# Kernel tuning notes

Measured on AMD Instinct MI355X. Metric: run time of the kernel, lower is better.

Reference implementation:

```python
import jax, jax.numpy as jnp
import numpy as np

H, KV, D, HID, Q, S = 16, 8, 128, 2048, 1024, 8192
CACHE_POS = 4096

def rotate_half(x, axis):
    x1, x2 = jnp.split(x, 2, axis)
    return jnp.concatenate((-x2, x1), axis=axis)

def setup_inputs() -> dict:
    key = jax.random.key(0)
    ks = jax.random.split(key, 12)
    hidden_states = jax.random.normal(ks[0], (1, HID, 1, Q), jnp.float32)
    # RoPE tables for the new token positions [CACHE_POS, CACHE_POS+Q)
    pos = jnp.arange(CACHE_POS, CACHE_POS + Q, dtype=jnp.float32)
    inv_freq = 1.0 / (10000.0 ** (jnp.arange(0, D, 2, dtype=jnp.float32) / D))
    ang = pos[:, None] * inv_freq[None, :]                      # (Q, D/2)
    cos = jnp.tile(jnp.cos(ang), (1, 2))[None, None]            # (1,1,Q,D)
    sin = jnp.tile(jnp.sin(ang), (1, 2))[None, None]
    cos_t = jnp.transpose(cos, (0, 1, 3, 2))                    # (1,1,D,Q)
    sin_t = jnp.transpose(sin, (0, 1, 3, 2))
    # causal mask over full cache: key slot s visible to query i iff s <= CACHE_POS + i
    k_idx = jnp.arange(S)[:, None]
    q_idx = jnp.arange(Q)[None, :]
    attention_mask = jnp.where(k_idx <= CACHE_POS + q_idx, 0.0, -1e9).astype(jnp.float32)[None, None]  # (1,1,S,Q)
    key_cache = 0.02 * jax.random.normal(ks[1], (1, KV, S, D), jnp.float32)
    value_cache = 0.02 * jax.random.normal(ks[2], (1, KV, S, D), jnp.float32)
    w = lambda k, shp: 0.02 * jax.random.normal(k, shp, jnp.float32)
    return dict(hidden_states=hidden_states, cos=cos, sin=sin, cos_t=cos_t, sin_t=sin_t,
                attention_mask=attention_mask, key_cache=key_cache, value_cache=value_cache,
                Wq=w(ks[3], (HID, HID)), bq=w(ks[4], (HID,)),
                Wk=w(ks[5], (KV * D, HID)), bk=w(ks[6], (KV * D,)),
                Wv=w(ks[7], (KV * D, HID)), bv=w(ks[8], (KV * D,)),
                Wo=w(ks[9], (HID, HID)), cache_position=CACHE_POS)

def reference(hidden_states, cos, sin, cos_t, sin_t, attention_mask,
              key_cache, value_cache, Wq, bq, Wk, bk, Wv, bv, Wo, cache_position):
    # 1x1-conv style projections on channels-first (1, C, 1, Q)
    q = jnp.einsum('oc,bcxq->boxq', Wq, hidden_states) + bq[None, :, None, None]
    k = jnp.einsum('oc,bcxq->boxq', Wk, hidden_states) + bk[None, :, None, None]
    v = jnp.einsum('oc,bcxq->boxq', Wv, hidden_states) + bv[None, :, None, None]
    q = q.reshape(1, H, D, Q)                                   # (1,H,D,Q)
    k = k.reshape(1, KV, D, Q).transpose(0, 1, 3, 2)            # (1,KV,Q,D)
    v = v.reshape(1, KV, D, Q).transpose(0, 1, 3, 2)
    # inline RoPE: q along head_dim axis (-2), k along last axis
    q = q * cos_t + rotate_half(q, -2) * sin_t
    k = k * cos + rotate_half(k, -1) * sin
    # KV-cache scatter at layer_idx=0, offset cache_position
    key_cache = jax.lax.dynamic_update_slice(key_cache, k, (0, 0, cache_position, 0))
    value_cache = jax.lax.dynamic_update_slice(value_cache, v, (0, 0, cache_position, 0))
    k_all = key_cache[0]                                        # (KV,S,D)
    v_all = value_cache[0]
    qg = q.reshape(KV, H // KV, D, Q)                           # GQA groups
    scores = jnp.einsum('ksd,kgdq->kgsq', k_all, qg) / jnp.sqrt(jnp.float32(D))
    scores = scores + attention_mask[0]                         # (1,S,Q) broadcast
    w = jax.nn.softmax(scores, axis=2)                          # softmax over cache slots
    out = jnp.einsum('kgsq,ksd->kgdq', w, v_all)                # (KV,G,D,Q)
    out = out.reshape(1, H * D, 1, Q)
    attn_output = jnp.einsum('oc,bcxq->boxq', Wo, out)
    return attn_output
```

## Files before the change

kernel.cpp:

```cpp
#include <hip/hip_runtime.h>

#define H_HEADS 16
#define KV_HEADS 8
#define DHEAD 128
#define HID 2048
#define NQ 1024
#define SCACHE 8192
#define CPOS 4096
#define SEFF 5120

typedef __attribute__((ext_vector_type(8))) __bf16 bf16x8;
typedef __attribute__((ext_vector_type(4))) float f32x4;
typedef unsigned short u16;
typedef unsigned int u32;

__device__ __forceinline__ u16 f2b(float f) {
  u32 u = __float_as_uint(f);
  u += 0x7fffu + ((u >> 16) & 1u);
  return (u16)(u >> 16);
}
__device__ __forceinline__ u16 f2b_t(float f) {
  return (u16)(__float_as_uint(f) >> 16);
}
__device__ __forceinline__ float b2f(u16 b) { return __uint_as_float(((u32)b) << 16); }
__device__ __forceinline__ u32 pk2(u16 a, u16 b) { return (u32)a | ((u32)b << 16); }
__device__ __forceinline__ uint2 f4b4(float4 v) {
  uint2 o;
  o.x = pk2(f2b(v.x), f2b(v.y));
  o.y = pk2(f2b(v.z), f2b(v.w));
  return o;
}

union U4 { uint4 v; u16 u[8]; };

__global__ void __launch_bounds__(256) k_conv_w(const float* __restrict__ Wq,
                                                const float* __restrict__ Wk,
                                                const float* __restrict__ Wv,
                                                u16* __restrict__ Wb) {
  int i = blockIdx.x * 256 + threadIdx.x;
  const float* src;
  int off;
  if (i < 1048576) { src = Wq; off = i; }
  else if (i < 1572864) { src = Wk; off = i - 1048576; }
  else { src = Wv; off = i - 1572864; }
  float4 v = ((const float4*)src)[off];
  *(uint2*)(Wb + (size_t)i * 4) = f4b4(v);
}

__global__ void __launch_bounds__(256) k_f32_to_bf16(const float* __restrict__ src,
                                                     u16* __restrict__ dst, int n4) {
  int i = blockIdx.x * 256 + threadIdx.x;
  if (i < n4) {
    float4 v = ((const float4*)src)[i];
    *(uint2*)(dst + (size_t)i * 4) = f4b4(v);
  }
}

__global__ void __launch_bounds__(256) k_transpose_h(const float* __restrict__ hid,
                                                     u16* __restrict__ hT) {
  __shared__ __align__(16) float ls[64 * 68];
  int t = threadIdx.x;
  int c0 = blockIdx.x * 64, q0 = blockIdx.y * 64;
#pragma unroll
  for (int it = 0; it < 4; ++it) {
    int c = it * 256 + t;
    int row = c >> 4, ch = c & 15;
    *(float4*)(ls + row * 68 + ch * 4) =
        *(const float4*)(hid + (size_t)(c0 + row) * NQ + q0 + ch * 4);
  }
  __syncthreads();
  int ql = t & 63, cch = t >> 6;
  u32 ob[8];
#pragma unroll
  for (int j = 0; j < 8; ++j)
    ob[j] = pk2(f2b(ls[(cch * 16 + 2 * j) * 68 + ql]), f2b(ls[(cch * 16 + 2 * j + 1) * 68 + ql]));
  uint4* dst = (uint4*)(hT + (size_t)(q0 + ql) * HID + c0 + cch * 16);
  dst[0] = make_uint4(ob[0], ob[1], ob[2], ob[3]);
  dst[1] = make_uint4(ob[4], ob[5], ob[6], ob[7]);
}

__global__ void __launch_bounds__(256) k_prep_vT(const float* __restrict__ vc,
                                                 u16* __restrict__ vT) {
  __shared__ __align__(16) float ls[64 * 132];
  int t = threadIdx.x;
  int s0 = blockIdx.x * 64;
  int kv = blockIdx.y;
#pragma unroll
  for (int it = 0; it < 8; ++it) {
    int c = it * 256 + t;
    int row = c >> 5, ch = c & 31;
    *(float4*)(ls + row * 132 + ch * 4) =
        *(const float4*)(vc + ((size_t)kv * SCACHE + s0 + row) * DHEAD + ch * 4);
  }
  __syncthreads();
  int d = t >> 1, sch = t & 1;
  u32 ob[16];
#pragma unroll
  for (int j = 0; j < 16; ++j)
    ob[j] = pk2(f2b(ls[(sch * 32 + 2 * j) * 132 + d]), f2b(ls[(sch * 32 + 2 * j + 1) * 132 + d]));
  uint4* dst = (uint4*)(vT + ((size_t)kv * DHEAD + d) * SEFF + s0 + sch * 32);
#pragma unroll
  for (int j = 0; j < 4; ++j)
    dst[j] = make_uint4(ob[4 * j], ob[4 * j + 1], ob[4 * j + 2], ob[4 * j + 3]);
}

__global__ void __launch_bounds__(256) k_conv_k(const float* __restrict__ kc,
                                                u16* __restrict__ kb) {
  int i = blockIdx.x * 256 + threadIdx.x;
  int kvi = i >> 17;
  int rem = i & 131071;
  float4 v = *(const float4*)(kc + (size_t)kvi * SCACHE * DHEAD + (size_t)rem * 4);
  *(uint2*)(kb + (size_t)kvi * SEFF * DHEAD + (size_t)rem * 4) = f4b4(v);
}

__global__ void __launch_bounds__(256) k_copy_vnew(const u16* __restrict__ qkv,
                                                   u16* __restrict__ vT) {
  int i = blockIdx.x * 256 + threadIdx.x;
  int row = i >> 7, ch = i & 127;
  *(uint4*)(vT + (size_t)row * SEFF + CPOS + ch * 8) =
      *(const uint4*)(qkv + (size_t)(3072 + row) * NQ + ch * 8);
}

__global__ void __launch_bounds__(256) k_rope_t(const u16* __restrict__ qkv,
                                                const float* __restrict__ cosb,
                                                const float* __restrict__ sinb,
                                                u16* __restrict__ qb,
                                                u16* __restrict__ kb) {
  __shared__ __align__(16) u16 ls[64 * 136];
  int t = threadIdx.x;
  int hh = blockIdx.x;
  int q0 = blockIdx.y * 64;
  bool isq = hh < 16;
  int rowbase = isq ? hh * DHEAD : HID + (hh - 16) * DHEAD;
#pragma unroll
  for (int it = 0; it < 4; ++it) {
    int c = it * 256 + t;
    int d = c >> 3, qc = (c & 7) * 8;
    U4 v;
    v.v = *(const uint4*)(qkv + (size_t)(rowbase + d) * NQ + q0 + qc);
#pragma unroll
    for (int e = 0; e < 8; ++e) ls[(qc + e) * 136 + d] = v.u[e];
  }
  __syncthreads();
  int ql = t & 63, hf = t >> 6;
  int q = q0 + ql;
  float scale = isq ? 0.08838834764831845f : 1.0f;
  u16* dst = isq ? (qb + ((size_t)hh * NQ + q) * DHEAD)
                 : (kb + ((size_t)(hh - 16) * SEFF + CPOS + q) * DHEAD);
#pragma unroll
  for (int g = 0; g < 4; ++g) {
    int d0 = hf * 32 + g * 8;
    U4 x, y;
    x.v = *(uint4*)(ls + ql * 136 + d0);
    y.v = *(uint4*)(ls + ql * 136 + (d0 ^ 64));
    float4 ca = *(const float4*)(cosb + (size_t)q * DHEAD + d0);
    float4 cb = *(const float4*)(cosb + (size_t)q * DHEAD + d0 + 4);
    float4 sa = *(const float4*)(sinb + (size_t)q * DHEAD + d0);
    float4 sb = *(const float4*)(sinb + (size_t)q * DHEAD + d0 + 4);
    float cs[8] = {ca.x, ca.y, ca.z, ca.w, cb.x, cb.y, cb.z, cb.w};
    float sn[8] = {sa.x, sa.y, sa.z, sa.w, sb.x, sb.y, sb.z, sb.w};
    float sgn = (d0 < 64) ? -1.0f : 1.0f;
    u32 ob[4];
#pragma unroll
    for (int e = 0; e < 4; ++e) {
      float r0 = (b2f(x.u[2 * e]) * cs[2 * e] + sgn * b2f(y.u[2 * e]) * sn[2 * e]) * scale;
      float r1 = (b2f(x.u[2 * e + 1]) * cs[2 * e + 1] + sgn * b2f(y.u[2 * e + 1]) * sn[2 * e + 1]) * scale;
      ob[e] = pk2(f2b(r0), f2b(r1));
    }
    *(uint4*)(dst + d0) = make_uint4(ob[0], ob[1], ob[2], ob[3]);
  }
}

__global__ void __launch_bounds__(256) k_gemm_qkv(
    const u16* __restrict__ Wb, const u16* __restrict__ hT, u16* __restrict__ qkv,
    const float* __restrict__ bq, const float* __restrict__ bk, const float* __restrict__ bv) {
  __shared__ __align__(16) u16 lsA[128 * 32];
  __shared__ __align__(16) u16 lsB[128 * 32];
  int t = threadIdx.x;
  int m0 = blockIdx.x * 128, n0 = blockIdx.y * 128;
  const u16* Abase = Wb + (size_t)m0 * HID;
  int lane = t & 63, wid = t >> 6;
  int quad = lane >> 4, l15 = lane & 15;
  int wr = wid >> 1, wc = wid & 1;
  f32x4 acc[4][4];
#pragma unroll
  for (int i = 0; i < 4; ++i)
#pragma unroll
    for (int j = 0; j < 4; ++j) acc[i][j] = (f32x4){0.f, 0.f, 0.f, 0.f};
  for (int kt = 0; kt < HID; kt += 32) {
    __syncthreads();
#pragma unroll
    for (int it = 0; it < 2; ++it) {
      int c = it * 256 + t;
      int row = c >> 2, ch = c & 3;
      *(uint4*)(lsA + row * 32 + ch * 8) =
          *(const uint4*)(Abase + (size_t)row * HID + kt + ch * 8);
      *(uint4*)(lsB + row * 32 + ch * 8) =
          *(const uint4*)(hT + (size_t)(n0 + row) * HID + kt + ch * 8);
    }
    __syncthreads();
    bf16x8 af[4], bfr[4];
#pragma unroll
    for (int i = 0; i < 4; ++i)
      af[i] = *(const bf16x8*)(lsA + (wr * 64 + i * 16 + l15) * 32 + quad * 8);
#pragma unroll
    for (int j = 0; j < 4; ++j)
      bfr[j] = *(const bf16x8*)(lsB + (wc * 64 + j * 16 + l15) * 32 + quad * 8);
#pragma unroll
    for (int i = 0; i < 4; ++i)
#pragma unroll
      for (int j = 0; j < 4; ++j)
        acc[i][j] = __builtin_amdgcn_mfma_f32_16x16x32_bf16(af[i], bfr[j], acc[i][j], 0, 0, 0);
  }
#pragma unroll
  for (int i = 0; i < 4; ++i) {
#pragma unroll
    for (int r = 0; r < 4; ++r) {
      int m = m0 + wr * 64 + i * 16 + quad * 4 + r;
      float bias = (m < 2048) ? bq[m] : ((m < 3072) ? bk[m - 2048] : bv[m - 3072]);
#pragma unroll
      for (int j = 0; j < 4; ++j) {
        int n = n0 + wc * 64 + j * 16 + l15;
        qkv[(size_t)m * NQ + n] = f2b(acc[i][j][r] + bias);
      }
    }
  }
}

__global__ void __launch_bounds__(512) k_flash(const u16* __restrict__ qb,
                                               const u16* __restrict__ kb,
                                               const u16* __restrict__ vT,
                                               u16* __restrict__ po,
                                               float* __restrict__ pm,
                                               float* __restrict__ pl) {
  __shared__ __align__(16) u16 lsK[64 * 136];
  __shared__ __align__(16) u16 lsV[144 * 68];
  __shared__ __align__(16) u16 lsP[8 * 16 * 68];
  int t = threadIdx.x;
  int h = blockIdx.x, qt = blockIdx.y, z = blockIdx.z;
  int kv = h >> 1;
  int q0 = qt * 128;
  int lane = t & 63, wid = t >> 6;
  int quad = lane >> 4, l15 = lane & 15;
  int qw = q0 + wid * 16;
  if (t < 128) {
    int row = 128 + (t >> 3), ch = t & 7;
    u32 fill = (row == 128) ? 0x3f803f80u : 0u;
    *(uint4*)(lsV + row * 68 + ch * 8) = make_uint4(fill, fill, fill, fill);
  }
  bf16x8 qf[4];
  const u16* qrow = qb + ((size_t)h * NQ + qw + l15) * DHEAD;
#pragma unroll
  for (int kc = 0; kc < 4; ++kc) qf[kc] = *(const bf16x8*)(qrow + kc * 32 + quad * 8);
  f32x4 oacc[9];
#pragma unroll
  for (int f = 0; f < 9; ++f) oacc[f] = (f32x4){0.f, 0.f, 0.f, 0.f};
  float m_run[4];
#pragma unroll
  for (int r = 0; r < 4; ++r) m_run[r] = -1e30f;
  u16* lsPw = lsP + wid * (16 * 68);
  int Svis = CPOS + q0 + 128;
  const u16* kbase = kb + (size_t)kv * SEFF * DHEAD;
  const u16* vbase = vT + (size_t)kv * DHEAD * SEFF;
  for (int s0 = z * 64; s0 < Svis; s0 += 256) {
#pragma unroll
    for (int it = 0; it < 2; ++it) {
      int c = it * 512 + t;
      int rowK = c >> 4, chK = c & 15;
      *(uint4*)(lsK + rowK * 136 + chK * 8) =
          *(const uint4*)(kbase + (size_t)(s0 + rowK) * DHEAD + chK * 8);
      int rowV = c >> 3, chV = c & 7;
      *(uint4*)(lsV + rowV * 68 + chV * 8) =
          *(const uint4*)(vbase + (size_t)rowV * SEFF + s0 + chV * 8);
    }
    __syncthreads();
    f32x4 sc[4];
#pragma unroll
    for (int js = 0; js < 4; ++js) {
      sc[js] = (f32x4){0.f, 0.f, 0.f, 0.f};
#pragma unroll
      for (int kc = 0; kc < 4; ++kc) {
        bf16x8 kf = *(const bf16x8*)(lsK + (js * 16 + l15) * 136 + kc * 32 + quad * 8);
        sc[js] = __builtin_amdgcn_mfma_f32_16x16x32_bf16(qf[kc], kf, sc[js], 0, 0, 0);
      }
    }
    if (s0 + 63 > CPOS + qw) {
#pragma unroll
      for (int r = 0; r < 4; ++r) {
        int lim = CPOS + qw + quad * 4 + r - s0;
#pragma unroll
        for (int js = 0; js < 4; ++js) {
          bool valid = (js * 16 + l15) <= lim;
          sc[js][r] = valid ? sc[js][r] : -1e30f;
        }
      }
    }
    float alpha[4];
#pragma unroll
    for (int r = 0; r < 4; ++r) {
      float mx = fmaxf(fmaxf(sc[0][r], sc[1][r]), fmaxf(sc[2][r], sc[3][r]));
      mx = fmaxf(mx, __shfl_xor(mx, 1, 64));
      mx = fmaxf(mx, __shfl_xor(mx, 2, 64));
      mx = fmaxf(mx, __shfl_xor(mx, 4, 64));
      mx = fmaxf(mx, __shfl_xor(mx, 8, 64));
      float mnew = fmaxf(m_run[r], mx);
      alpha[r] = __expf(m_run[r] - mnew);
      m_run[r] = mnew;
#pragma unroll
      for (int js = 0; js < 4; ++js) {
        float p = __expf(sc[js][r] - mnew);
        lsPw[(quad * 4 + r) * 68 + js * 16 + l15] = f2b_t(p);
      }
    }
#pragma unroll
    for (int f = 0; f < 9; ++f)
#pragma unroll
      for (int r = 0; r < 4; ++r) oacc[f][r] *= alpha[r];
    bf16x8 pf[2];
#pragma unroll
    for (int ks = 0; ks < 2; ++ks)
      pf[ks] = *(const bf16x8*)(lsPw + l15 * 68 + ks * 32 + quad * 8);
#pragma unroll
    for (int f = 0; f < 9; ++f) {
#pragma unroll
      for (int ks = 0; ks < 2; ++ks) {
        bf16x8 vf = *(const bf16x8*)(lsV + (f * 16 + l15) * 68 + ks * 32 + quad * 8);
        oacc[f] = __builtin_amdgcn_mfma_f32_16x16x32_bf16(pf[ks], vf, oacc[f], 0, 0, 0);
      }
    }
    __syncthreads();
  }
  int p = (h * 8 + qt) * 4 + z;
#pragma unroll
  for (int r = 0; r < 4; ++r) {
    int qloc = wid * 16 + quad * 4 + r;
    if (l15 == 0) {
      pm[(size_t)p * 128 + qloc] = m_run[r];
      pl[(size_t)p * 128 + qloc] = oacc[8][r];
    }
#pragma unroll
    for (int f = 0; f < 8; ++f)
      po[(size_t)p * 16384 + qloc * 128 + f * 16 + l15] = f2b(oacc[f][r]);
  }
}

__global__ void __launch_bounds__(256) k_combine(const u16* __restrict__ po,
                                                 const float* __restrict__ pm,
                                                 const float* __restrict__ pl,
                                                 u16* __restrict__ outT) {
  int t = threadIdx.x;
  int h = blockIdx.x, qt = blockIdx.y;
  int q = qt * 64 + (t >> 2);
  int dq = (t & 3) * 32;
  int pb = (h * 8 + (q >> 7)) * 4;
  int ql = q & 127;
  float m0 = pm[(size_t)(pb + 0) * 128 + ql];
  float m1 = pm[(size_t)(pb + 1) * 128 + ql];
  float m2 = pm[(size_t)(pb + 2) * 128 + ql];
  float m3 = pm[(size_t)(pb + 3) * 128 + ql];
  float M = fmaxf(fmaxf(m0, m1), fmaxf(m2, m3));
  float w[4] = {__expf(m0 - M), __expf(m1 - M), __expf(m2 - M), __expf(m3 - M)};
  float L = 0.f;
#pragma unroll
  for (int zz = 0; zz < 4; ++zz) L += w[zz] * pl[(size_t)(pb + zz) * 128 + ql];
  float acc[32];
#pragma unroll
  for (int e = 0; e < 32; ++e) acc[e] = 0.f;
#pragma unroll
  for (int zz = 0; zz < 4; ++zz) {
    const u16* src = po + (size_t)(pb + zz) * 16384 + ql * 128 + dq;
#pragma unroll
    for (int j = 0; j < 4; ++j) {
      U4 v;
      v.v = *(const uint4*)(src + j * 8);
#pragma unroll
      for (int e = 0; e < 8; ++e) acc[j * 8 + e] += w[zz] * b2f(v.u[e]);
    }
  }
  float inv = 1.0f / L;
  u16* dst = outT + (size_t)q * HID + h * DHEAD + dq;
#pragma unroll
  for (int j = 0; j < 4; ++j) {
    u32 ob[4];
#pragma unroll
    for (int e = 0; e < 4; ++e)
      ob[e] = pk2(f2b(acc[j * 8 + 2 * e] * inv), f2b(acc[j * 8 + 2 * e + 1] * inv));
    *(uint4*)(dst + j * 8) = make_uint4(ob[0], ob[1], ob[2], ob[3]);
  }
}

__global__ void __launch_bounds__(256) k_gemm_bt(const u16* __restrict__ A,
                                                 const u16* __restrict__ BT,
                                                 float* __restrict__ C) {
  __shared__ __align__(16) u16 lsA[128 * 32];
  __shared__ __align__(16) u16 lsB[64 * 32];
  int t = threadIdx.x;
  int m0 = blockIdx.x * 128, n0 = blockIdx.y * 64;
  const u16* Abase = A + (size_t)m0 * HID;
  const u16* Bbase = BT + (size_t)n0 * HID;
  int lane = t & 63, wid = t >> 6;
  int quad = lane >> 4, l15 = lane & 15;
  int wr = wid >> 1, wc = wid & 1;
  f32x4 acc[4][2];
#pragma unroll
  for (int i = 0; i < 4; ++i)
#pragma unroll
    for (int j = 0; j < 2; ++j) acc[i][j] = (f32x4){0.f, 0.f, 0.f, 0.f};
  for (int kt = 0; kt < HID; kt += 32) {
    __syncthreads();
#pragma unroll
    for (int it = 0; it < 2; ++it) {
      int c = it * 256 + t;
      int row = c >> 2, ch = c & 3;
      *(uint4*)(lsA + row * 32 + ch * 8) =
          *(const uint4*)(Abase + (size_t)row * HID + kt + ch * 8);
    }
    {
      int row = t >> 2, ch = t & 3;
      *(uint4*)(lsB + row * 32 + ch * 8) =
          *(const uint4*)(Bbase + (size_t)row * HID + kt + ch * 8);
    }
    __syncthreads();
    bf16x8 af[4], bfr[2];
#pragma unroll
    for (int i = 0; i < 4; ++i)
      af[i] = *(const bf16x8*)(lsA + (wr * 64 + i * 16 + l15) * 32 + quad * 8);
#pragma unroll
    for (int j = 0; j < 2; ++j)
      bfr[j] = *(const bf16x8*)(lsB + (wc * 32 + j * 16 + l15) * 32 + quad * 8);
#pragma unroll
    for (int i = 0; i < 4; ++i)
#pragma unroll
      for (int j = 0; j < 2; ++j)
        acc[i][j] = __builtin_amdgcn_mfma_f32_16x16x32_bf16(af[i], bfr[j], acc[i][j], 0, 0, 0);
  }
#pragma unroll
  for (int i = 0; i < 4; ++i)
#pragma unroll
    for (int r = 0; r < 4; ++r) {
      int m = m0 + wr * 64 + i * 16 + quad * 4 + r;
#pragma unroll
      for (int j = 0; j < 2; ++j) {
        int n = n0 + wc * 32 + j * 16 + l15;
        C[(size_t)m * NQ + n] = acc[i][j][r];
      }
    }
}

extern "C" void kernel_launch(void* const* d_in, const int* in_sizes, int n_in,
                              void* d_out, int out_size, void* d_ws, size_t ws_size,
                              hipStream_t stream) {
  (void)in_sizes; (void)n_in; (void)out_size; (void)ws_size;
  const float* hidden = (const float*)d_in[0];
  const float* cosb = (const float*)d_in[1];
  const float* sinb = (const float*)d_in[2];
  const float* kcache = (const float*)d_in[6];
  const float* vcache = (const float*)d_in[7];
  const float* Wq = (const float*)d_in[8];
  const float* bq = (const float*)d_in[9];
  const float* Wk = (const float*)d_in[10];
  const float* bk = (const float*)d_in[11];
  const float* Wv = (const float*)d_in[12];
  const float* bv = (const float*)d_in[13];
  const float* Wo = (const float*)d_in[14];

  char* ws = (char*)d_ws;
  u16* qkv = (u16*)(ws);
  u16* outT = (u16*)(ws + 8388608);
  u16* hT = outT;
  u16* vT = (u16*)(ws + 12582912);
  u16* Wob = vT;
  u16* kb = (u16*)(ws + 23068672);
  u16* qb = (u16*)(ws + 33554432);
  u16* Wb = (u16*)(ws + 12582912);
  u16* po = (u16*)(ws + 37748736);
  float* pm = (float*)(ws + 54525952);
  float* pl = (float*)(ws + 54788096);
  float* outb = (float*)d_out;

  k_conv_w<<<8192, 256, 0, stream>>>(Wq, Wk, Wv, Wb);
  k_transpose_h<<<dim3(32, 16), 256, 0, stream>>>(hidden, hT);
  k_gemm_qkv<<<dim3(32, 8), 256, 0, stream>>>(Wb, hT, qkv, bq, bk, bv);
  k_prep_vT<<<dim3(64, 8), 256, 0, stream>>>(vcache, vT);
  k_conv_k<<<4096, 256, 0, stream>>>(kcache, kb);
  k_rope_t<<<dim3(24, 16), 256, 0, stream>>>(qkv, cosb, sinb, qb, kb);
  k_copy_vnew<<<512, 256, 0, stream>>>(qkv, vT);
  k_flash<<<dim3(16, 8, 4), 512, 0, stream>>>(qb, kb, vT, po, pm, pl);
  k_f32_to_bf16<<<4096, 256, 0, stream>>>(Wo, Wob, 1048576);
  k_combine<<<dim3(16, 16), 256, 0, stream>>>(po, pm, pl, outT);
  k_gemm_bt<<<dim3(16, 16), 256, 0, stream>>>(Wob, outT, outb);
}
```

Before: 389.1 us.

## Give each flash-attention wave two query tiles and halve the block size

Each wave in the flash kernel now handles 32 query rows as two 16-row groups, and the block drops from 512 to 256 threads. Every K and V fragment read from LDS therefore feeds two MFMAs instead of one, cutting LDS traffic per unit of compute. The row-sum is now taken with a separate MFMA against a ones vector instead of a padded ninth V tile. LDS row strides also change (68 to 72). In exchange, register pressure per thread rises and fewer waves per block are available to hide global-load latency.

```diff
diff --git a/kernel.cpp b/kernel.cpp
--- a/kernel.cpp
+++ b/kernel.cpp
@@ -227,120 +227,159 @@
   }
 }
 
-__global__ void __launch_bounds__(512) k_flash(const u16* __restrict__ qb,
+__global__ void __launch_bounds__(256) k_flash(const u16* __restrict__ qb,
                                                const u16* __restrict__ kb,
                                                const u16* __restrict__ vT,
                                                u16* __restrict__ po,
                                                float* __restrict__ pm,
                                                float* __restrict__ pl) {
   __shared__ __align__(16) u16 lsK[64 * 136];
-  __shared__ __align__(16) u16 lsV[144 * 68];
-  __shared__ __align__(16) u16 lsP[8 * 16 * 68];
+  __shared__ __align__(16) u16 lsV[128 * 72];
+  __shared__ __align__(16) u16 lsP[4 * 32 * 72];
   int t = threadIdx.x;
   int h = blockIdx.x, qt = blockIdx.y, z = blockIdx.z;
   int kv = h >> 1;
   int q0 = qt * 128;
   int lane = t & 63, wid = t >> 6;
   int quad = lane >> 4, l15 = lane & 15;
-  int qw = q0 + wid * 16;
-  if (t < 128) {
-    int row = 128 + (t >> 3), ch = t & 7;
-    u32 fill = (row == 128) ? 0x3f803f80u : 0u;
-    *(uint4*)(lsV + row * 68 + ch * 8) = make_uint4(fill, fill, fill, fill);
-  }
-  bf16x8 qf[4];
-  const u16* qrow = qb + ((size_t)h * NQ + qw + l15) * DHEAD;
-#pragma unroll
-  for (int kc = 0; kc < 4; ++kc) qf[kc] = *(const bf16x8*)(qrow + kc * 32 + quad * 8);
-  f32x4 oacc[9];
-#pragma unroll
-  for (int f = 0; f < 9; ++f) oacc[f] = (f32x4){0.f, 0.f, 0.f, 0.f};
-  float m_run[4];
-#pragma unroll
-  for (int r = 0; r < 4; ++r) m_run[r] = -1e30f;
-  u16* lsPw = lsP + wid * (16 * 68);
+  int qw = q0 + wid * 32;
+
+  union { u16 u[8]; bf16x8 v; } onesu;
+#pragma unroll
+  for (int e = 0; e < 8; ++e) onesu.u[e] = 0x3f80;
+  bf16x8 onesf = onesu.v;
+
+  bf16x8 qf0[4], qf1[4];
+  const u16* qrow0 = qb + ((size_t)h * NQ + qw + l15) * DHEAD;
+  const u16* qrow1 = qrow0 + (size_t)16 * DHEAD;
+#pragma unroll
+  for (int kc = 0; kc < 4; ++kc) {
+    qf0[kc] = *(const bf16x8*)(qrow0 + kc * 32 + quad * 8);
+    qf1[kc] = *(const bf16x8*)(qrow1 + kc * 32 + quad * 8);
+  }
+  f32x4 oacc[2][8];
+#pragma unroll
+  for (int g = 0; g < 2; ++g)
+#pragma unroll
+    for (int f = 0; f < 8; ++f) oacc[g][f] = (f32x4){0.f, 0.f, 0.f, 0.f};
+  f32x4 lacc[2];
+  lacc[0] = (f32x4){0.f, 0.f, 0.f, 0.f};
+  lacc[1] = (f32x4){0.f, 0.f, 0.f, 0.f};
+  float m_run[2][4];
+#pragma unroll
+  for (int g = 0; g < 2; ++g)
+#pragma unroll
+    for (int r = 0; r < 4; ++r) m_run[g][r] = -1e30f;
+  u16* lsPw = lsP + wid * (32 * 72);
   int Svis = CPOS + q0 + 128;
   const u16* kbase = kb + (size_t)kv * SEFF * DHEAD;
   const u16* vbase = vT + (size_t)kv * DHEAD * SEFF;
   for (int s0 = z * 64; s0 < Svis; s0 += 256) {
 #pragma unroll
-    for (int it = 0; it < 2; ++it) {
-      int c = it * 512 + t;
+    for (int it = 0; it < 4; ++it) {
+      int c = it * 256 + t;
       int rowK = c >> 4, chK = c & 15;
       *(uint4*)(lsK + rowK * 136 + chK * 8) =
           *(const uint4*)(kbase + (size_t)(s0 + rowK) * DHEAD + chK * 8);
       int rowV = c >> 3, chV = c & 7;
-      *(uint4*)(lsV + rowV * 68 + chV * 8) =
+      *(uint4*)(lsV + rowV * 72 + chV * 8) =
           *(const uint4*)(vbase + (size_t)rowV * SEFF + s0 + chV * 8);
     }
     __syncthreads();
-    f32x4 sc[4];
+    f32x4 sc[2][4];
+#pragma unroll
+    for (int g = 0; g < 2; ++g)
+#pragma unroll
+      for (int js = 0; js < 4; ++js) sc[g][js] = (f32x4){0.f, 0.f, 0.f, 0.f};
 #pragma unroll
     for (int js = 0; js < 4; ++js) {
-      sc[js] = (f32x4){0.f, 0.f, 0.f, 0.f};
 #pragma unroll
       for (int kc = 0; kc < 4; ++kc) {
         bf16x8 kf = *(const bf16x8*)(lsK + (js * 16 + l15) * 136 + kc * 32 + quad * 8);
-        sc[js] = __builtin_amdgcn_mfma_f32_16x16x32_bf16(qf[kc], kf, sc[js], 0, 0, 0);
-      }
-    }
-    if (s0 + 63 > CPOS + qw) {
+        sc[0][js] = __builtin_amdgcn_mfma_f32_16x16x32_bf16(qf0[kc], kf, sc[0][js], 0, 0, 0);
+        sc[1][js] = __builtin_amdgcn_mfma_f32_16x16x32_bf16(qf1[kc], kf, sc[1][js], 0, 0, 0);
+      }
+    }
+#pragma unroll
+    for (int g = 0; g < 2; ++g) {
+      int qwg = qw + g * 16;
+      if (s0 + 63 > CPOS + qwg) {
+#pragma unroll
+        for (int r = 0; r < 4; ++r) {
+          int lim = CPOS + qwg + quad * 4 + r - s0;
+#pragma unroll
+          for (int js = 0; js < 4; ++js) {
+            bool valid = (js * 16 + l15) <= lim;
+            sc[g][js][r] = valid ? sc[g][js][r] : -1e30f;
+          }
+        }
+      }
+    }
+    float alpha[2][4];
+#pragma unroll
+    for (int g = 0; g < 2; ++g) {
 #pragma unroll
       for (int r = 0; r < 4; ++r) {
-        int lim = CPOS + qw + quad * 4 + r - s0;
+        float mx = fmaxf(fmaxf(sc[g][0][r], sc[g][1][r]), fmaxf(sc[g][2][r], sc[g][3][r]));
+        mx = fmaxf(mx, __shfl_xor(mx, 1, 64));
+        mx = fmaxf(mx, __shfl_xor(mx, 2, 64));
+        mx = fmaxf(mx, __shfl_xor(mx, 4, 64));
+        mx = fmaxf(mx, __shfl_xor(mx, 8, 64));
+        float mnew = fmaxf(m_run[g][r], mx);
+        alpha[g][r] = __expf(m_run[g][r] - mnew);
+        m_run[g][r] = mnew;
 #pragma unroll
         for (int js = 0; js < 4; ++js) {
-          bool valid = (js * 16 + l15) <= lim;
-          sc[js][r] = valid ? sc[js][r] : -1e30f;
+          float p = __expf(sc[g][js][r] - mnew);
+          lsPw[(g * 16 + quad * 4 + r) * 72 + js * 16 + l15] = f2b_t(p);
         }
       }
     }
-    float alpha[4];
+#pragma unroll
+    for (int g = 0; g < 2; ++g) {
+#pragma unroll
+      for (int f = 0; f < 8; ++f)
+#pragma unroll
+        for (int r = 0; r < 4; ++r) oacc[g][f][r] *= alpha[g][r];
+#pragma unroll
+      for (int r = 0; r < 4; ++r) lacc[g][r] *= alpha[g][r];
+    }
+    bf16x8 pf0[2], pf1[2];
+#pragma unroll
+    for (int ks = 0; ks < 2; ++ks) {
+      pf0[ks] = *(const bf16x8*)(lsPw + l15 * 72 + ks * 32 + quad * 8);
+      pf1[ks] = *(const bf16x8*)(lsPw + (16 + l15) * 72 + ks * 32 + quad * 8);
+    }
+#pragma unroll
+    for (int f = 0; f < 8; ++f) {
+#pragma unroll
+      for (int ks = 0; ks < 2; ++ks) {
+        bf16x8 vf = *(const bf16x8*)(lsV + (f * 16 + l15) * 72 + ks * 32 + quad * 8);
+        oacc[0][f] = __builtin_amdgcn_mfma_f32_16x16x32_bf16(pf0[ks], vf, oacc[0][f], 0, 0, 0);
+        oacc[1][f] = __builtin_amdgcn_mfma_f32_16x16x32_bf16(pf1[ks], vf, oacc[1][f], 0, 0, 0);
+      }
+    }
+#pragma unroll
+    for (int ks = 0; ks < 2; ++ks) {
+      lacc[0] = __builtin_amdgcn_mfma_f32_16x16x32_bf16(pf0[ks], onesf, lacc[0], 0, 0, 0);
+      lacc[1] = __builtin_amdgcn_mfma_f32_16x16x32_bf16(pf1[ks], onesf, lacc[1], 0, 0, 0);
+    }
+    __syncthreads();
+  }
+  int p = (h * 8 + qt) * 4 + z;
+#pragma unroll
+  for (int g = 0; g < 2; ++g) {
 #pragma unroll
     for (int r = 0; r < 4; ++r) {
-      float mx = fmaxf(fmaxf(sc[0][r], sc[1][r]), fmaxf(sc[2][r], sc[3][r]));
-      mx = fmaxf(mx, __shfl_xor(mx, 1, 64));
-      mx = fmaxf(mx, __shfl_xor(mx, 2, 64));
-      mx = fmaxf(mx, __shfl_xor(mx, 4, 64));
-      mx = fmaxf(mx, __shfl_xor(mx, 8, 64));
-      float mnew = fmaxf(m_run[r], mx);
-      alpha[r] = __expf(m_run[r] - mnew);
-      m_run[r] = mnew;
-#pragma unroll
-      for (int js = 0; js < 4; ++js) {
-        float p = __expf(sc[js][r] - mnew);
-        lsPw[(quad * 4 + r) * 68 + js * 16 + l15] = f2b_t(p);
-      }
-    }
-#pragma unroll
-    for (int f = 0; f < 9; ++f)
-#pragma unroll
-      for (int r = 0; r < 4; ++r) oacc[f][r] *= alpha[r];
-    bf16x8 pf[2];
-#pragma unroll
-    for (int ks = 0; ks < 2; ++ks)
-      pf[ks] = *(const bf16x8*)(lsPw + l15 * 68 + ks * 32 + quad * 8);
-#pragma unroll
-    for (int f = 0; f < 9; ++f) {
-#pragma unroll
-      for (int ks = 0; ks < 2; ++ks) {
-        bf16x8 vf = *(const bf16x8*)(lsV + (f * 16 + l15) * 68 + ks * 32 + quad * 8);
-        oacc[f] = __builtin_amdgcn_mfma_f32_16x16x32_bf16(pf[ks], vf, oacc[f], 0, 0, 0);
-      }
-    }
-    __syncthreads();
-  }
-  int p = (h * 8 + qt) * 4 + z;
-#pragma unroll
-  for (int r = 0; r < 4; ++r) {
-    int qloc = wid * 16 + quad * 4 + r;
-    if (l15 == 0) {
-      pm[(size_t)p * 128 + qloc] = m_run[r];
-      pl[(size_t)p * 128 + qloc] = oacc[8][r];
-    }
-#pragma unroll
-    for (int f = 0; f < 8; ++f)
-      po[(size_t)p * 16384 + qloc * 128 + f * 16 + l15] = f2b(oacc[f][r]);
+      int qloc = wid * 32 + g * 16 + quad * 4 + r;
+      if (l15 == 0) {
+        pm[(size_t)p * 128 + qloc] = m_run[g][r];
+        pl[(size_t)p * 128 + qloc] = lacc[g][r];
+      }
+#pragma unroll
+      for (int f = 0; f < 8; ++f)
+        po[(size_t)p * 16384 + qloc * 128 + f * 16 + l15] = f2b(oacc[g][f][r]);
+    }
   }
 }
 
@@ -485,7 +524,7 @@
   k_conv_k<<<4096, 256, 0, stream>>>(kcache, kb);
   k_rope_t<<<dim3(24, 16), 256, 0, stream>>>(qkv, cosb, sinb, qb, kb);
   k_copy_vnew<<<512, 256, 0, stream>>>(qkv, vT);
-  k_flash<<<dim3(16, 8, 4), 512, 0, stream>>>(qb, kb, vT, po, pm, pl);
+  k_flash<<<dim3(16, 8, 4), 256, 0, stream>>>(qb, kb, vT, po, pm, pl);
   k_f32_to_bf16<<<4096, 256, 0, stream>>>(Wo, Wob, 1048576);
   k_combine<<<dim3(16, 16), 256, 0, stream>>>(po, pm, pl, outT);
   k_gemm_bt<<<dim3(16, 16), 256, 0, stream>>>(Wob, outT, outb);
```

New measurement: 477.1 us. +22.6%, slower.

## Prefetch next K/V tile into registers and compute row sums with register ones

Applied to the files above, without the earlier changes.

The flash attention loop now loads the next K and V tiles from global memory into registers while the current tile is being computed, then writes them to LDS at the start of the next iteration. This is meant to hide global load latency behind the MFMA work. The row-sum accumulator now uses a register constant of bf16 ones instead of an extra LDS row block, and the LDS strides for V and P change from 68 to 72. The cost is extra registers for the prefetch buffers and a different LDS bank pattern.

```diff
diff --git a/kernel.cpp b/kernel.cpp
--- a/kernel.cpp
+++ b/kernel.cpp
@@ -234,8 +234,8 @@
                                                float* __restrict__ pm,
                                                float* __restrict__ pl) {
   __shared__ __align__(16) u16 lsK[64 * 136];
-  __shared__ __align__(16) u16 lsV[144 * 68];
-  __shared__ __align__(16) u16 lsP[8 * 16 * 68];
+  __shared__ __align__(16) u16 lsV[128 * 72];
+  __shared__ __align__(16) u16 lsP[8 * 16 * 72];
   int t = threadIdx.x;
   int h = blockIdx.x, qt = blockIdx.y, z = blockIdx.z;
   int kv = h >> 1;
@@ -243,37 +243,52 @@
   int lane = t & 63, wid = t >> 6;
   int quad = lane >> 4, l15 = lane & 15;
   int qw = q0 + wid * 16;
-  if (t < 128) {
-    int row = 128 + (t >> 3), ch = t & 7;
-    u32 fill = (row == 128) ? 0x3f803f80u : 0u;
-    *(uint4*)(lsV + row * 68 + ch * 8) = make_uint4(fill, fill, fill, fill);
-  }
+
+  union { u16 u[8]; bf16x8 v; } onesu;
+#pragma unroll
+  for (int e = 0; e < 8; ++e) onesu.u[e] = 0x3f80;
+  bf16x8 onesf = onesu.v;
+
   bf16x8 qf[4];
   const u16* qrow = qb + ((size_t)h * NQ + qw + l15) * DHEAD;
 #pragma unroll
   for (int kc = 0; kc < 4; ++kc) qf[kc] = *(const bf16x8*)(qrow + kc * 32 + quad * 8);
-  f32x4 oacc[9];
-#pragma unroll
-  for (int f = 0; f < 9; ++f) oacc[f] = (f32x4){0.f, 0.f, 0.f, 0.f};
+  f32x4 oacc[8];
+#pragma unroll
+  for (int f = 0; f < 8; ++f) oacc[f] = (f32x4){0.f, 0.f, 0.f, 0.f};
+  f32x4 lacc = (f32x4){0.f, 0.f, 0.f, 0.f};
   float m_run[4];
 #pragma unroll
   for (int r = 0; r < 4; ++r) m_run[r] = -1e30f;
-  u16* lsPw = lsP + wid * (16 * 68);
+  u16* lsPw = lsP + wid * (16 * 72);
   int Svis = CPOS + q0 + 128;
   const u16* kbase = kb + (size_t)kv * SEFF * DHEAD;
   const u16* vbase = vT + (size_t)kv * DHEAD * SEFF;
+
+  int rK = t >> 4, cK = (t & 15) * 8;
+  int rV = t >> 3, cV = (t & 7) * 8;
+  uint4 pk0, pk1, pv0, pv1;
+  {
+    int s0 = z * 64;
+    pk0 = *(const uint4*)(kbase + (size_t)(s0 + rK) * DHEAD + cK);
+    pk1 = *(const uint4*)(kbase + (size_t)(s0 + 32 + rK) * DHEAD + cK);
+    pv0 = *(const uint4*)(vbase + (size_t)rV * SEFF + s0 + cV);
+    pv1 = *(const uint4*)(vbase + (size_t)(64 + rV) * SEFF + s0 + cV);
+  }
   for (int s0 = z * 64; s0 < Svis; s0 += 256) {
-#pragma unroll
-    for (int it = 0; it < 2; ++it) {
-      int c = it * 512 + t;
-      int rowK = c >> 4, chK = c & 15;
-      *(uint4*)(lsK + rowK * 136 + chK * 8) =
-          *(const uint4*)(kbase + (size_t)(s0 + rowK) * DHEAD + chK * 8);
-      int rowV = c >> 3, chV = c & 7;
-      *(uint4*)(lsV + rowV * 68 + chV * 8) =
-          *(const uint4*)(vbase + (size_t)rowV * SEFF + s0 + chV * 8);
-    }
     __syncthreads();
+    *(uint4*)(lsK + rK * 136 + cK) = pk0;
+    *(uint4*)(lsK + (32 + rK) * 136 + cK) = pk1;
+    *(uint4*)(lsV + rV * 72 + cV) = pv0;
+    *(uint4*)(lsV + (64 + rV) * 72 + cV) = pv1;
+    __syncthreads();
+    int sn = s0 + 256;
+    if (sn < Svis) {
+      pk0 = *(const uint4*)(kbase + (size_t)(sn + rK) * DHEAD + cK);
+      pk1 = *(const uint4*)(kbase + (size_t)(sn + 32 + rK) * DHEAD + cK);
+      pv0 = *(const uint4*)(vbase + (size_t)rV * SEFF + sn + cV);
+      pv1 = *(const uint4*)(vbase + (size_t)(64 + rV) * SEFF + sn + cV);
+    }
     f32x4 sc[4];
 #pragma unroll
     for (int js = 0; js < 4; ++js) {
@@ -309,26 +324,30 @@
 #pragma unroll
       for (int js = 0; js < 4; ++js) {
         float p = __expf(sc[js][r] - mnew);
-        lsPw[(quad * 4 + r) * 68 + js * 16 + l15] = f2b_t(p);
+        lsPw[(quad * 4 + r) * 72 + js * 16 + l15] = f2b_t(p);
       }
     }
 #pragma unroll
-    for (int f = 0; f < 9; ++f)
+    for (int f = 0; f < 8; ++f)
 #pragma unroll
       for (int r = 0; r < 4; ++r) oacc[f][r] *= alpha[r];
+#pragma unroll
+    for (int r = 0; r < 4; ++r) lacc[r] *= alpha[r];
     bf16x8 pf[2];
 #pragma unroll
     for (int ks = 0; ks < 2; ++ks)
-      pf[ks] = *(const bf16x8*)(lsPw + l15 * 68 + ks * 32 + quad * 8);
-#pragma unroll
-    for (int f = 0; f < 9; ++f) {
+      pf[ks] = *(const bf16x8*)(lsPw + l15 * 72 + ks * 32 + quad * 8);
+#pragma unroll
+    for (int f = 0; f < 8; ++f) {
 #pragma unroll
       for (int ks = 0; ks < 2; ++ks) {
-        bf16x8 vf = *(const bf16x8*)(lsV + (f * 16 + l15) * 68 + ks * 32 + quad * 8);
+        bf16x8 vf = *(const bf16x8*)(lsV + (f * 16 + l15) * 72 + ks * 32 + quad * 8);
         oacc[f] = __builtin_amdgcn_mfma_f32_16x16x32_bf16(pf[ks], vf, oacc[f], 0, 0, 0);
       }
     }
-    __syncthreads();
+#pragma unroll
+    for (int ks = 0; ks < 2; ++ks)
+      lacc = __builtin_amdgcn_mfma_f32_16x16x32_bf16(pf[ks], onesf, lacc, 0, 0, 0);
   }
   int p = (h * 8 + qt) * 4 + z;
 #pragma unroll
@@ -336,7 +355,7 @@
     int qloc = wid * 16 + quad * 4 + r;
     if (l15 == 0) {
       pm[(size_t)p * 128 + qloc] = m_run[r];
-      pl[(size_t)p * 128 + qloc] = oacc[8][r];
+      pl[(size_t)p * 128 + qloc] = lacc[r];
     }
 #pragma unroll
     for (int f = 0; f < 8; ++f)
```

After: 365.4 us. 1.06x faster.
